# Kernel optimization log

Measured on AMD Instinct MI355X. Metric: run time of the kernel, lower is better.

## Reference

```python
import jax, jax.numpy as jnp
import numpy as np

N = 100000   # nodes
E = 1600000  # edges (avg degree 16)
D = 128      # input feature dim
H = 128      # Config.hidden_dim
G = 64       # graphs in batch
OUT = 2      # output classes


def setup_inputs() -> dict:
    key = jax.random.key(0)
    ks = jax.random.split(key, 12)
    s = 0.05
    return {
        "x": jax.random.normal(ks[0], (N, D), dtype=jnp.float32),
        "edge_index": jax.random.randint(ks[1], (2, E), 0, N),
        "batch": jnp.sort(jax.random.randint(ks[2], (N,), 0, G)),
        "W1": jax.random.normal(ks[3], (H, D), dtype=jnp.float32) * s,
        "b1": jnp.zeros((H,), jnp.float32),
        "W2": jax.random.normal(ks[4], (H, H), dtype=jnp.float32) * s,
        "b2": jnp.zeros((H,), jnp.float32),
        "Wf1": jax.random.normal(ks[5], (H, H), dtype=jnp.float32) * s,
        "bf1": jnp.zeros((H,), jnp.float32),
        "Wf2": jax.random.normal(ks[6], (OUT, H), dtype=jnp.float32) * s,
        "bf2": jnp.zeros((OUT,), jnp.float32),
    }


def _gnn_layer(x, src, dst, W, b):
    # message(x_j) = Linear(x[src]); linear commutes with gather, so transform
    # node features once (N rows) instead of per-edge (E rows): same math.
    xw = x @ W.T + b                                   # [N, H]
    msg = xw[src]                                      # [E, H] gather
    summed = jax.ops.segment_sum(msg, dst, num_segments=N)            # [N, H]
    cnt = jax.ops.segment_sum(jnp.ones((src.shape[0],), x.dtype), dst,
                              num_segments=N)                          # [N]
    return summed / jnp.maximum(cnt, 1.0)[:, None]     # scatter-mean (0 for deg-0)


def reference(x, edge_index, batch, W1, b1, W2, b2, Wf1, bf1, Wf2, bf2):
    src, dst = edge_index[0], edge_index[1]
    h = jax.nn.relu(_gnn_layer(x, src, dst, W1, b1))
    h = jax.nn.relu(_gnn_layer(h, src, dst, W2, b2))
    g = jax.ops.segment_max(h, batch, num_segments=G)  # global_max_pool [G, H]
    z = jax.nn.relu(g @ Wf1.T + bf1)                   # fc (dropout = identity, eval)
    z = z @ Wf2.T + bf2                                # [G, OUT]
    return jax.nn.log_softmax(z, axis=1)
```

## Files before the change

### kernel.cpp

```cpp
#include <hip/hip_runtime.h>
#include <hip/hip_fp16.h>
#include <math.h>


#define SPLIT 16
#define BUCKET_SHIFT 8
#define BUCKET_SIZE 256
#define MAXBUCK 512
#define BIN_CHUNK 4096
#define CAP 4608
#define LSTR 136

typedef _Float16 half8 __attribute__((ext_vector_type(8)));
typedef _Float16 half4v __attribute__((ext_vector_type(4)));
typedef float floatx4 __attribute__((ext_vector_type(4)));
typedef float floatx2 __attribute__((ext_vector_type(2)));

__global__ void k_init(int* bcur, int* gstart, int* gend, int G, int nbuck) {
    int i = threadIdx.x;
    if (i < nbuck) bcur[i] = i * CAP;
    if (i < G) { gstart[i] = 0; gend[i] = 0; }
}

__global__ void k_bin(const int* __restrict__ src, const int* __restrict__ dst,
                      int* __restrict__ bcur, int* __restrict__ staging,
                      int E, int nbuck) {
    __shared__ int lh[MAXBUCK];
    __shared__ int lbase[MAXBUCK];
    __shared__ int lc[MAXBUCK];
    for (int i = threadIdx.x; i < nbuck; i += blockDim.x) { lh[i] = 0; lc[i] = 0; }
    __syncthreads();
    int base = blockIdx.x * BIN_CHUNK;
    int end = min(base + BIN_CHUNK, E);
    for (int e = base + threadIdx.x; e < end; e += blockDim.x)
        atomicAdd(&lh[dst[e] >> BUCKET_SHIFT], 1);
    __syncthreads();
    for (int i = threadIdx.x; i < nbuck; i += blockDim.x)
        if (lh[i]) lbase[i] = atomicAdd(&bcur[i], lh[i]);
    __syncthreads();
    for (int e = base + threadIdx.x; e < end; e += blockDim.x) {
        int d = dst[e];
        int b = d >> BUCKET_SHIFT;
        int pos = lbase[b] + atomicAdd(&lc[b], 1);
        if (pos < (b + 1) * CAP)
            staging[pos] = src[e] | ((d & (BUCKET_SIZE - 1)) << 24);
    }
}

__global__ __launch_bounds__(BUCKET_SIZE) void k_bcsr(
        const int* __restrict__ staging, const int* __restrict__ bcur,
        int* __restrict__ esrc, int* __restrict__ rowstart,
        int* __restrict__ deg, int N) {
    __shared__ int lh[BUCKET_SIZE];
    __shared__ int lrs[BUCKET_SIZE];
    __shared__ int lcur[BUCKET_SIZE];
    int b = blockIdx.x;
    int s = b * CAP;
    int e = min(bcur[b], s + CAP);
    int t = threadIdx.x;
    lh[t] = 0;
    __syncthreads();
    for (int i = s + t; i < e; i += BUCKET_SIZE)
        atomicAdd(&lh[((unsigned)staging[i]) >> 24], 1);
    __syncthreads();
    int v = lh[t];
    lrs[t] = v;
    __syncthreads();
    for (int off = 1; off < BUCKET_SIZE; off <<= 1) {
        int x = (t >= off) ? lrs[t - off] : 0;
        __syncthreads();
        lrs[t] += x;
        __syncthreads();
    }
    int excl = lrs[t] - v;
    int node = b * BUCKET_SIZE + t;
    if (node < N) { rowstart[node] = s + excl; deg[node] = v; }
    lcur[t] = excl;
    __syncthreads();
    for (int i = s + t; i < e; i += BUCKET_SIZE) {
        int p = staging[i];
        int local = ((unsigned)p) >> 24;
        int pos = atomicAdd(&lcur[local], 1);
        esrc[s + pos] = p & 0xFFFFFF;
    }
}

template <typename T>
__global__ __launch_bounds__(512) void k_gemm(const T* __restrict__ in,
                                              const float* __restrict__ W,
                                              const float* __restrict__ bias,
                                              unsigned char* __restrict__ out8,
                                              int N) {
    __shared__ _Float16 sX[128 * LSTR];
    __shared__ _Float16 sW[128 * LSTR];
    int t = threadIdx.x;
    int n0 = blockIdx.x * 128;

    #pragma unroll
    for (int it = 0; it < 8; ++it) {
        int lin = it * 512 + t;
        int r = lin >> 5;
        int c = (lin & 31) * 4;
        half4v xh;
        int n = n0 + r;
        if (n < N) {
            if constexpr (sizeof(T) == 4) {
                float4 xv = *(const float4*)((const float*)in + (size_t)n * 128 + c);
                xh = half4v{ (_Float16)xv.x, (_Float16)xv.y, (_Float16)xv.z, (_Float16)xv.w };
            } else {
                xh = *(const half4v*)((const _Float16*)in + (size_t)n * 128 + c);
            }
        } else {
            xh = half4v{ 0, 0, 0, 0 };
        }
        float4 wv = *(const float4*)(W + r * 128 + c);
        half4v wh = { (_Float16)wv.x, (_Float16)wv.y, (_Float16)wv.z, (_Float16)wv.w };
        *(half4v*)&sX[r * LSTR + c] = xh;
        *(half4v*)&sW[r * LSTR + c] = wh;
    }
    __syncthreads();

    int w = t >> 6;
    int lane = t & 63;
    int quad = lane >> 4;
    int lrow = lane & 15;

    floatx4 acc[8];
    #pragma unroll
    for (int i = 0; i < 8; ++i) acc[i] = {0.f, 0.f, 0.f, 0.f};

    int arow = (w * 16 + lrow) * LSTR + quad * 8;
    #pragma unroll
    for (int k0 = 0; k0 < 128; k0 += 32) {
        half8 a = *(const half8*)&sX[arow + k0];
        #pragma unroll
        for (int ht = 0; ht < 8; ++ht) {
            half8 b = *(const half8*)&sW[(ht * 16 + lrow) * LSTR + quad * 8 + k0];
            acc[ht] = __builtin_amdgcn_mfma_f32_16x16x32_f16(a, b, acc[ht], 0, 0, 0);
        }
    }

    #pragma unroll
    for (int ht = 0; ht < 8; ++ht) {
        int h = ht * 16 + lrow;
        float bv = bias[h];
        #pragma unroll
        for (int r = 0; r < 4; ++r) {
            int node = n0 + w * 16 + quad * 4 + r;
            if (node < N) {
                float v = acc[ht][r] + bv;
                int pk = __builtin_amdgcn_cvt_pk_fp8_f32(v, v, 0, false);
                out8[(size_t)node * 128 + h] = (unsigned char)(pk & 0xFF);
            }
        }
    }
}

__global__ __launch_bounds__(256) void k_agg(const unsigned char* __restrict__ in8,
                                             const int* __restrict__ esrc,
                                             const int* __restrict__ rowstart,
                                             const int* __restrict__ deg,
                                             _Float16* __restrict__ outh, int N) {
    int lane = threadIdx.x & 31;
    int grp  = threadIdx.x >> 5;
    int node = blockIdx.x * 8 + grp;
    if (node >= N) return;
    int start = rowstart[node];
    int d = deg[node];
    const unsigned* in1 = (const unsigned*)in8;
    float4 a0 = make_float4(0.f, 0.f, 0.f, 0.f);
    float4 a1 = make_float4(0.f, 0.f, 0.f, 0.f);
    float4 a2 = make_float4(0.f, 0.f, 0.f, 0.f);
    float4 a3 = make_float4(0.f, 0.f, 0.f, 0.f);
    int i = 0;
    for (; i + 4 <= d; i += 4) {
        unsigned u0 = in1[(size_t)esrc[start + i]     * 32 + lane];
        unsigned u1 = in1[(size_t)esrc[start + i + 1] * 32 + lane];
        unsigned u2 = in1[(size_t)esrc[start + i + 2] * 32 + lane];
        unsigned u3 = in1[(size_t)esrc[start + i + 3] * 32 + lane];
        floatx2 l0 = __builtin_amdgcn_cvt_pk_f32_fp8(u0, false);
        floatx2 h0 = __builtin_amdgcn_cvt_pk_f32_fp8(u0, true);
        floatx2 l1 = __builtin_amdgcn_cvt_pk_f32_fp8(u1, false);
        floatx2 h1 = __builtin_amdgcn_cvt_pk_f32_fp8(u1, true);
        floatx2 l2 = __builtin_amdgcn_cvt_pk_f32_fp8(u2, false);
        floatx2 h2 = __builtin_amdgcn_cvt_pk_f32_fp8(u2, true);
        floatx2 l3 = __builtin_amdgcn_cvt_pk_f32_fp8(u3, false);
        floatx2 h3 = __builtin_amdgcn_cvt_pk_f32_fp8(u3, true);
        a0.x += l0.x; a0.y += l0.y; a0.z += h0.x; a0.w += h0.y;
        a1.x += l1.x; a1.y += l1.y; a1.z += h1.x; a1.w += h1.y;
        a2.x += l2.x; a2.y += l2.y; a2.z += h2.x; a2.w += h2.y;
        a3.x += l3.x; a3.y += l3.y; a3.z += h3.x; a3.w += h3.y;
    }
    for (; i < d; ++i) {
        unsigned u = in1[(size_t)esrc[start + i] * 32 + lane];
        floatx2 lo = __builtin_amdgcn_cvt_pk_f32_fp8(u, false);
        floatx2 hi = __builtin_amdgcn_cvt_pk_f32_fp8(u, true);
        a0.x += lo.x; a0.y += lo.y; a0.z += hi.x; a0.w += hi.y;
    }
    float4 acc;
    acc.x = (a0.x + a1.x) + (a2.x + a3.x);
    acc.y = (a0.y + a1.y) + (a2.y + a3.y);
    acc.z = (a0.z + a1.z) + (a2.z + a3.z);
    acc.w = (a0.w + a1.w) + (a2.w + a3.w);
    float dm = fmaxf((float)d, 1.0f);
    half4v r = { (_Float16)fmaxf(acc.x / dm, 0.f),
                 (_Float16)fmaxf(acc.y / dm, 0.f),
                 (_Float16)fmaxf(acc.z / dm, 0.f),
                 (_Float16)fmaxf(acc.w / dm, 0.f) };
    *(half4v*)(outh + (size_t)node * 128 + lane * 4) = r;
}

__global__ void k_bounds(const int* __restrict__ batch, int* __restrict__ gstart,
                         int* __restrict__ gend, int N) {
    int n = blockIdx.x * blockDim.x + threadIdx.x;
    if (n >= N) return;
    int b = batch[n];
    if (n == 0 || batch[n - 1] != b) gstart[b] = n;
    if (n == N - 1 || batch[n + 1] != b) gend[b] = n + 1;
}

__global__ void k_pool1(const _Float16* __restrict__ h, const int* __restrict__ gstart,
                        const int* __restrict__ gend, float* __restrict__ pm, int G) {
    int g = blockIdx.x / SPLIT;
    int c = blockIdx.x % SPLIT;
    int t = threadIdx.x;
    int s = gstart[g], e = gend[g];
    int len = e - s;
    int chunk = (len + SPLIT - 1) / SPLIT;
    int lo = s + c * chunk;
    int hi = min(lo + chunk, e);
    float m = -INFINITY;
    for (int n = lo; n < hi; ++n)
        m = fmaxf(m, (float)h[(size_t)n * 128 + t]);
    pm[((size_t)g * SPLIT + c) * 128 + t] = m;
}

__global__ void k_fc(const float* __restrict__ pm,
                     const float* __restrict__ Wf1, const float* __restrict__ bf1,
                     const float* __restrict__ Wf2, const float* __restrict__ bf2,
                     float* __restrict__ out) {
    __shared__ float sg[128];
    __shared__ float sz[128];
    __shared__ float so[2];
    int g = blockIdx.x;
    int t = threadIdx.x;
    float m = -INFINITY;
    #pragma unroll
    for (int c = 0; c < SPLIT; ++c)
        m = fmaxf(m, pm[((size_t)g * SPLIT + c) * 128 + t]);
    sg[t] = m;
    __syncthreads();
    float z = bf1[t];
    #pragma unroll 4
    for (int d = 0; d < 128; ++d)
        z += sg[d] * Wf1[t * 128 + d];
    sz[t] = fmaxf(z, 0.f);
    __syncthreads();
    if (t < 2) {
        float o = bf2[t];
        for (int d = 0; d < 128; ++d)
            o += sz[d] * Wf2[t * 128 + d];
        so[t] = o;
    }
    __syncthreads();
    if (t == 0) {
        float a = so[0], b = so[1];
        float mx = fmaxf(a, b);
        float ls = mx + logf(expf(a - mx) + expf(b - mx));
        out[g * 2 + 0] = a - ls;
        out[g * 2 + 1] = b - ls;
    }
}

extern "C" void kernel_launch(void* const* d_in, const int* in_sizes, int n_in,
                              void* d_out, int out_size, void* d_ws, size_t ws_size,
                              hipStream_t stream) {
    const float* x   = (const float*)d_in[0];
    const int*   ei  = (const int*)d_in[1];
    const int* batch = (const int*)d_in[2];
    const float* W1  = (const float*)d_in[3];
    const float* b1  = (const float*)d_in[4];
    const float* W2  = (const float*)d_in[5];
    const float* b2  = (const float*)d_in[6];
    const float* Wf1 = (const float*)d_in[7];
    const float* bf1 = (const float*)d_in[8];
    const float* Wf2 = (const float*)d_in[9];
    const float* bf2 = (const float*)d_in[10];

    int N = in_sizes[2];
    int E = in_sizes[1] / 2;
    int G = out_size / 2;
    const int* src = ei;
    const int* dst = ei + E;
    int nbuck = (N + BUCKET_SIZE - 1) / BUCKET_SIZE;

    char* p = (char*)d_ws;
    auto alloc = [&](size_t bytes) -> char* {
        char* r = p;
        p += (bytes + 255) & ~(size_t)255;
        return r;
    };
    unsigned char* A = (unsigned char*)alloc((size_t)N * 128);
    _Float16* B    = (_Float16*)alloc((size_t)N * 128 * 2);
    int* deg       = (int*)alloc((size_t)N * 4);
    int* rowstart  = (int*)alloc((size_t)N * 4);
    int* esrc      = (int*)alloc((size_t)nbuck * CAP * 4);
    int* staging   = (int*)alloc((size_t)nbuck * CAP * 4);
    int* bcur      = (int*)alloc((MAXBUCK + 2) * 4);
    int* gstart    = (int*)alloc((size_t)G * 4);
    int* gend      = (int*)alloc((size_t)G * 4);
    float* pm      = (float*)alloc((size_t)G * SPLIT * 128 * 4);

    int nchunk = (E + BIN_CHUNK - 1) / BIN_CHUNK;

    k_init<<<1, MAXBUCK, 0, stream>>>(bcur, gstart, gend, G, nbuck);
    k_bin<<<nchunk, 256, 0, stream>>>(src, dst, bcur, staging, E, nbuck);
    k_bcsr<<<nbuck, BUCKET_SIZE, 0, stream>>>(staging, bcur, esrc, rowstart, deg, N);
    k_bounds<<<(N + 255) / 256, 256, 0, stream>>>(batch, gstart, gend, N);

    k_gemm<float><<<(N + 127) / 128, 512, 0, stream>>>(x, W1, b1, A, N);
    k_agg<<<(N + 7) / 8, 256, 0, stream>>>(A, esrc, rowstart, deg, B, N);
    k_gemm<_Float16><<<(N + 127) / 128, 512, 0, stream>>>(B, W2, b2, A, N);
    k_agg<<<(N + 7) / 8, 256, 0, stream>>>(A, esrc, rowstart, deg, B, N);
    k_pool1<<<G * SPLIT, 128, 0, stream>>>(B, gstart, gend, pm, G);
    k_fc<<<G, 128, 0, stream>>>(pm, Wf1, bf1, Wf2, bf2, (float*)d_out);
}
```

Baseline: 309.2 us.

## Assign one node per wavefront in aggregation and fold bounds into binning

The aggregation kernel now gives each 64-lane wavefront a single node, with its two 32-lane halves gathering alternate neighbour rows. The halves are combined with a cross-half shuffle at the end. Degree and row start become wave-uniform scalars via readfirstlane, which removes divergence from two nodes with different degrees sharing one wave. The graph-boundary computation moves into the binning kernel to save a launch. That fold depends on the binning grid having at least N threads, which holds for the current E/N ratio but is fragile.

```diff
diff --git a/kernel.cpp b/kernel.cpp
--- a/kernel.cpp
+++ b/kernel.cpp
@@ -24,10 +24,17 @@
 
 __global__ void k_bin(const int* __restrict__ src, const int* __restrict__ dst,
                       int* __restrict__ bcur, int* __restrict__ staging,
-                      int E, int nbuck) {
+                      const int* __restrict__ batch, int* __restrict__ gstart,
+                      int* __restrict__ gend, int E, int N, int nbuck) {
     __shared__ int lh[MAXBUCK];
     __shared__ int lbase[MAXBUCK];
     __shared__ int lc[MAXBUCK];
+    int gid = blockIdx.x * blockDim.x + threadIdx.x;
+    if (gid < N) {
+        int b = batch[gid];
+        if (gid == 0 || batch[gid - 1] != b) gstart[b] = gid;
+        if (gid == N - 1 || batch[gid + 1] != b) gend[b] = gid + 1;
+    }
     for (int i = threadIdx.x; i < nbuck; i += blockDim.x) { lh[i] = 0; lc[i] = 0; }
     __syncthreads();
     int base = blockIdx.x * BIN_CHUNK;
@@ -161,62 +168,61 @@
                                              const int* __restrict__ rowstart,
                                              const int* __restrict__ deg,
                                              _Float16* __restrict__ outh, int N) {
-    int lane = threadIdx.x & 31;
-    int grp  = threadIdx.x >> 5;
-    int node = blockIdx.x * 8 + grp;
+    int wv = __builtin_amdgcn_readfirstlane(threadIdx.x >> 6);
+    int node = blockIdx.x * 4 + wv;
     if (node >= N) return;
-    int start = rowstart[node];
-    int d = deg[node];
-    const unsigned* in1 = (const unsigned*)in8;
-    float4 a0 = make_float4(0.f, 0.f, 0.f, 0.f);
-    float4 a1 = make_float4(0.f, 0.f, 0.f, 0.f);
-    float4 a2 = make_float4(0.f, 0.f, 0.f, 0.f);
-    float4 a3 = make_float4(0.f, 0.f, 0.f, 0.f);
+    int lane = threadIdx.x & 63;
+    int half = lane >> 5;
+    unsigned voff = (lane & 31) * 4;
+    int start = __builtin_amdgcn_readfirstlane(rowstart[node]);
+    int d = __builtin_amdgcn_readfirstlane(deg[node]);
+
+    floatx2 a0lo = {0.f, 0.f}, a0hi = {0.f, 0.f};
+    floatx2 a1lo = {0.f, 0.f}, a1hi = {0.f, 0.f};
     int i = 0;
     for (; i + 4 <= d; i += 4) {
-        unsigned u0 = in1[(size_t)esrc[start + i]     * 32 + lane];
-        unsigned u1 = in1[(size_t)esrc[start + i + 1] * 32 + lane];
-        unsigned u2 = in1[(size_t)esrc[start + i + 2] * 32 + lane];
-        unsigned u3 = in1[(size_t)esrc[start + i + 3] * 32 + lane];
-        floatx2 l0 = __builtin_amdgcn_cvt_pk_f32_fp8(u0, false);
-        floatx2 h0 = __builtin_amdgcn_cvt_pk_f32_fp8(u0, true);
-        floatx2 l1 = __builtin_amdgcn_cvt_pk_f32_fp8(u1, false);
-        floatx2 h1 = __builtin_amdgcn_cvt_pk_f32_fp8(u1, true);
-        floatx2 l2 = __builtin_amdgcn_cvt_pk_f32_fp8(u2, false);
-        floatx2 h2 = __builtin_amdgcn_cvt_pk_f32_fp8(u2, true);
-        floatx2 l3 = __builtin_amdgcn_cvt_pk_f32_fp8(u3, false);
-        floatx2 h3 = __builtin_amdgcn_cvt_pk_f32_fp8(u3, true);
-        a0.x += l0.x; a0.y += l0.y; a0.z += h0.x; a0.w += h0.y;
-        a1.x += l1.x; a1.y += l1.y; a1.z += h1.x; a1.w += h1.y;
-        a2.x += l2.x; a2.y += l2.y; a2.z += h2.x; a2.w += h2.y;
-        a3.x += l3.x; a3.y += l3.y; a3.z += h3.x; a3.w += h3.y;
-    }
-    for (; i < d; ++i) {
-        unsigned u = in1[(size_t)esrc[start + i] * 32 + lane];
-        floatx2 lo = __builtin_amdgcn_cvt_pk_f32_fp8(u, false);
-        floatx2 hi = __builtin_amdgcn_cvt_pk_f32_fp8(u, true);
-        a0.x += lo.x; a0.y += lo.y; a0.z += hi.x; a0.w += hi.y;
-    }
-    float4 acc;
-    acc.x = (a0.x + a1.x) + (a2.x + a3.x);
-    acc.y = (a0.y + a1.y) + (a2.y + a3.y);
-    acc.z = (a0.z + a1.z) + (a2.z + a3.z);
-    acc.w = (a0.w + a1.w) + (a2.w + a3.w);
-    float dm = fmaxf((float)d, 1.0f);
-    half4v r = { (_Float16)fmaxf(acc.x / dm, 0.f),
-                 (_Float16)fmaxf(acc.y / dm, 0.f),
-                 (_Float16)fmaxf(acc.z / dm, 0.f),
-                 (_Float16)fmaxf(acc.w / dm, 0.f) };
-    *(half4v*)(outh + (size_t)node * 128 + lane * 4) = r;
-}
-
-__global__ void k_bounds(const int* __restrict__ batch, int* __restrict__ gstart,
-                         int* __restrict__ gend, int N) {
-    int n = blockIdx.x * blockDim.x + threadIdx.x;
-    if (n >= N) return;
-    int b = batch[n];
-    if (n == 0 || batch[n - 1] != b) gstart[b] = n;
-    if (n == N - 1 || batch[n + 1] != b) gend[b] = n + 1;
+        int e0 = esrc[start + i];
+        int e1 = esrc[start + i + 1];
+        int e2 = esrc[start + i + 2];
+        int e3 = esrc[start + i + 3];
+        unsigned s01 = (unsigned)(half ? e1 : e0);
+        unsigned s23 = (unsigned)(half ? e3 : e2);
+        unsigned u0 = *(const unsigned*)(in8 + ((size_t)s01 << 7) + voff);
+        unsigned u1 = *(const unsigned*)(in8 + ((size_t)s23 << 7) + voff);
+        a0lo += __builtin_amdgcn_cvt_pk_f32_fp8(u0, false);
+        a0hi += __builtin_amdgcn_cvt_pk_f32_fp8(u0, true);
+        a1lo += __builtin_amdgcn_cvt_pk_f32_fp8(u1, false);
+        a1hi += __builtin_amdgcn_cvt_pk_f32_fp8(u1, true);
+    }
+    for (; i + 2 <= d; i += 2) {
+        int e0 = esrc[start + i];
+        int e1 = esrc[start + i + 1];
+        unsigned s01 = (unsigned)(half ? e1 : e0);
+        unsigned u0 = *(const unsigned*)(in8 + ((size_t)s01 << 7) + voff);
+        a0lo += __builtin_amdgcn_cvt_pk_f32_fp8(u0, false);
+        a0hi += __builtin_amdgcn_cvt_pk_f32_fp8(u0, true);
+    }
+    if (i < d) {
+        int e0 = esrc[start + i];
+        unsigned u0 = *(const unsigned*)(in8 + ((size_t)e0 << 7) + voff);
+        floatx2 lo = __builtin_amdgcn_cvt_pk_f32_fp8(u0, false);
+        floatx2 hi = __builtin_amdgcn_cvt_pk_f32_fp8(u0, true);
+        if (half == 0) { a0lo += lo; a0hi += hi; }
+    }
+    floatx2 slo = a0lo + a1lo;
+    floatx2 shi = a0hi + a1hi;
+    float c0 = slo.x + __shfl_down(slo.x, 32);
+    float c1 = slo.y + __shfl_down(slo.y, 32);
+    float c2 = shi.x + __shfl_down(shi.x, 32);
+    float c3 = shi.y + __shfl_down(shi.y, 32);
+    if (half == 0) {
+        float dm = fmaxf((float)d, 1.0f);
+        half4v r = { (_Float16)fmaxf(c0 / dm, 0.f),
+                     (_Float16)fmaxf(c1 / dm, 0.f),
+                     (_Float16)fmaxf(c2 / dm, 0.f),
+                     (_Float16)fmaxf(c3 / dm, 0.f) };
+        *(half4v*)(outh + (size_t)node * 128 + (lane & 31) * 4) = r;
+    }
 }
 
 __global__ void k_pool1(const _Float16* __restrict__ h, const int* __restrict__ gstart,
@@ -314,14 +320,14 @@
     int nchunk = (E + BIN_CHUNK - 1) / BIN_CHUNK;
 
     k_init<<<1, MAXBUCK, 0, stream>>>(bcur, gstart, gend, G, nbuck);
-    k_bin<<<nchunk, 256, 0, stream>>>(src, dst, bcur, staging, E, nbuck);
+    k_bin<<<nchunk, 256, 0, stream>>>(src, dst, bcur, staging, batch,
+                                      gstart, gend, E, N, nbuck);
     k_bcsr<<<nbuck, BUCKET_SIZE, 0, stream>>>(staging, bcur, esrc, rowstart, deg, N);
-    k_bounds<<<(N + 255) / 256, 256, 0, stream>>>(batch, gstart, gend, N);
 
     k_gemm<float><<<(N + 127) / 128, 512, 0, stream>>>(x, W1, b1, A, N);
-    k_agg<<<(N + 7) / 8, 256, 0, stream>>>(A, esrc, rowstart, deg, B, N);
+    k_agg<<<(N + 3) / 4, 256, 0, stream>>>(A, esrc, rowstart, deg, B, N);
     k_gemm<_Float16><<<(N + 127) / 128, 512, 0, stream>>>(B, W2, b2, A, N);
-    k_agg<<<(N + 7) / 8, 256, 0, stream>>>(A, esrc, rowstart, deg, B, N);
+    k_agg<<<(N + 3) / 4, 256, 0, stream>>>(A, esrc, rowstart, deg, B, N);
     k_pool1<<<G * SPLIT, 128, 0, stream>>>(B, gstart, gend, pm, G);
     k_fc<<<G, 128, 0, stream>>>(pm, Wf1, bf1, Wf2, bf2, (float*)d_out);
 }
```

Result: slower. 315.4 us (+2.0%).
